# Kernel optimization log

Measured on AMD Instinct MI355X. Metric: run time of the kernel, lower is better.

The kernel has to match this reference:

```python
import jax, jax.numpy as jnp
import numpy as np

BLOCK = 32           # sparsity_config.block
STRIDE_BLOCKS = 4    # stride 128 // block 32
B, H, L, HD = 2, 16, 4096, 64


def _make_fixed_layout(nb, bs):
    """DeepSpeed 'fixed' unidirectional layout, numverts=vertsize=1 (same for all heads)."""
    lay = np.zeros((nb, nb), dtype=np.int64)
    # local: lower-triangular within each stride window
    for i in range(0, nb, bs):
        for j in range(i, i + bs):
            lay[j, i:j + 1] = 1
    # global: vertical stripe at column offset bs-1 of every window, causal (col < row)
    start = bs - 1
    for i in range(nb):
        for j in range(start, i, bs):
            lay[i, j] = 1
    rows, cols = np.nonzero(lay)  # sorted by row
    return jnp.asarray(rows, jnp.int32), jnp.asarray(cols, jnp.int32)


def setup_inputs() -> dict:
    key = jax.random.key(0)
    kq, kk, kv = jax.random.split(key, 3)
    query = jax.random.normal(kq, (B, H, L, HD), jnp.float32)
    key_t = jax.random.normal(kk, (B, H, L, HD), jnp.float32)
    value = jax.random.normal(kv, (B, H, L, HD), jnp.float32)
    rows, cols = _make_fixed_layout(L // BLOCK, STRIDE_BLOCKS)
    return {"query": query, "key": key_t, "value": value,
            "rows": rows, "cols": cols, "block": BLOCK}


def reference(query, key, value, rows, cols, block):
    b, h, l, hd = query.shape
    nb = l // block
    scale = float(hd) ** (-0.5)
    # [nb, B, H, block, hd] with block-row axis leading for gather/scatter
    qb = jnp.moveaxis(query.reshape(b, h, nb, block, hd), 2, 0)
    kb = jnp.moveaxis(key.reshape(b, h, nb, block, hd), 2, 0)
    vb = jnp.moveaxis(value.reshape(b, h, nb, block, hd), 2, 0)
    # sdd: scores only on active blocks -> [nnz, B, H, block, block]
    s = jnp.einsum('nbhqd,nbhkd->nbhqk', qb[rows], kb[cols]) * scale
    # block-sparse softmax over each query row (segment reduce over blocks sharing a row)
    m_blk = s.max(-1)  # [nnz, B, H, block]
    row_max = jnp.full((nb, b, h, block), -jnp.inf, s.dtype).at[rows].max(m_blk)
    e = jnp.exp(s - row_max[rows][..., None])
    denom = jnp.zeros((nb, b, h, block), s.dtype).at[rows].add(e.sum(-1))
    p = e / denom[rows][..., None]
    # dsd: probs @ value, scatter-add into block rows
    ob = jnp.zeros((nb, b, h, block, hd), s.dtype).at[rows].add(
        jnp.einsum('nbhqk,nbhkd->nbhqd', p, vb[cols]))
    return jnp.moveaxis(ob, 0, 2).reshape(b, h, l, hd)
```

## Files before the change

kernel.cpp:

```cpp
#include <hip/hip_runtime.h>
#include <math.h>

#define BH    32
#define LSEQ  4096
#define HD    64
#define BLK   32
#define NB    128
#define NWIN  32
#define QSCALE 0.18033688011112042f

#define KSTR 34
#define VSTR 17

#define RAW_BARRIER() asm volatile("s_waitcnt lgkmcnt(0)\n\ts_barrier" ::: "memory")

typedef _Float16 h2  __attribute__((ext_vector_type(2)));
typedef _Float16 h8  __attribute__((ext_vector_type(8)));
typedef float    f16v __attribute__((ext_vector_type(16)));

static __device__ __forceinline__ h2 pk(float a, float b) {
    return __builtin_bit_cast(h2, __builtin_amdgcn_cvt_pkrtz(a, b));
}
static __device__ __forceinline__ unsigned pku(float a, float b) {
    return __builtin_bit_cast(unsigned, __builtin_amdgcn_cvt_pkrtz(a, b));
}
static __device__ __forceinline__ short h16(float x) {
    return __builtin_bit_cast(short, (_Float16)x);
}
static __device__ __forceinline__ h8 mk8(h2 a, h2 b, h2 c, h2 d) {
    h8 r;
    r[0] = a[0]; r[1] = a[1]; r[2] = b[0]; r[3] = b[1];
    r[4] = c[0]; r[5] = c[1]; r[6] = d[0]; r[7] = d[1];
    return r;
}

__global__ __launch_bounds__(256)
void sparse_attn_noshfl(const float* __restrict__ Q, const float* __restrict__ K,
                        const float* __restrict__ V, float* __restrict__ out)
{
    const int id = (int)blockIdx.x;
    const int bh = id & 31;
    const int p  = id >> 5;

    const int t    = (int)threadIdx.x;
    const int d    = t >> 6;
    const int lane = t & 63;
    const int l31  = lane & 31;
    const int h    = lane >> 5;

    __shared__ __align__(16) unsigned kbuf[2][BLK * KSTR];
    __shared__ __align__(16) unsigned vbuf[2][HD * VSTR];

    const size_t base = (size_t)bh * (LSEQ * HD);

    const int srow = t >> 3;
    const int sdg  = t & 7;
    const int vslot = (srow & 19) | ((srow & 4) << 1) | ((srow & 8) >> 1);

    const float* kgb = K + base + (size_t)srow * HD + sdg * 8;
    const float* vgb = V + base + (size_t)srow * HD + sdg * 8;

    float4 kA, kB, vA, vB;

    auto loadR = [&](int w, int j) {
        const int col = (j < w) ? (4 * j + 3) : (4 * w + (j - w));
        const size_t off = (size_t)col * (BLK * HD);
        kA = *(const float4*)(kgb + off);
        kB = *(const float4*)(kgb + off + 4);
        vA = *(const float4*)(vgb + off);
        vB = *(const float4*)(vgb + off + 4);
    };
    auto writeL = [&](int b) {
        uint2 w0, w1;
        w0.x = pku(kA.x, kA.y); w0.y = pku(kA.z, kA.w);
        w1.x = pku(kB.x, kB.y); w1.y = pku(kB.z, kB.w);
        *(uint2*)&kbuf[b][srow * KSTR + sdg * 4]     = w0;
        *(uint2*)&kbuf[b][srow * KSTR + sdg * 4 + 2] = w1;
        short* vs = (short*)&vbuf[b][0];
        const int vd0 = sdg * 8;
        vs[(vd0 + 0) * (2 * VSTR) + vslot] = h16(vA.x);
        vs[(vd0 + 1) * (2 * VSTR) + vslot] = h16(vA.y);
        vs[(vd0 + 2) * (2 * VSTR) + vslot] = h16(vA.z);
        vs[(vd0 + 3) * (2 * VSTR) + vslot] = h16(vA.w);
        vs[(vd0 + 4) * (2 * VSTR) + vslot] = h16(vB.x);
        vs[(vd0 + 5) * (2 * VSTR) + vslot] = h16(vB.y);
        vs[(vd0 + 6) * (2 * VSTR) + vslot] = h16(vB.z);
        vs[(vd0 + 7) * (2 * VSTR) + vslot] = h16(vB.w);
    };

    int pb = 0;
    loadR(p, 0);

    for (int ph = 0; ph < 2; ++ph) {
        const int w = ph ? (31 - p) : p;
        const int r = 4 * w + d;
        const int n = w + 4;

        const float* qp = Q + base + (size_t)(r * BLK + l31) * HD + 8 * h;
        h8 qf[4];
#pragma unroll
        for (int tt = 0; tt < 4; ++tt) {
            float4 a = *(const float4*)(qp + 16 * tt);
            float4 b = *(const float4*)(qp + 16 * tt + 4);
            qf[tt] = mk8(pk(a.x * QSCALE, a.y * QSCALE), pk(a.z * QSCALE, a.w * QSCALE),
                         pk(b.x * QSCALE, b.y * QSCALE), pk(b.z * QSCALE, b.w * QSCALE));
        }

        f16v o0 = {}, o1 = {};
        float2 ls2 = make_float2(0.0f, 0.0f);

        for (int j = 0; j < n; ++j, pb ^= 1) {
            writeL(pb);
            if (j + 1 < n)      loadR(w, j + 1);
            else if (ph == 0)   loadR(31 - p, 0);
            RAW_BARRIER();

            if (j < w || (j - w) <= d) {
                const unsigned* kb = kbuf[pb];
                const unsigned* vb = vbuf[pb];

                f16v st = {};
#pragma unroll
                for (int tt = 0; tt < 4; ++tt) {
                    const int kw = l31 * KSTR + 8 * tt + 4 * h;
                    uint2 u0 = *(const uint2*)&kb[kw];
                    uint2 u1 = *(const uint2*)&kb[kw + 2];
                    uint4 uu; uu.x = u0.x; uu.y = u0.y; uu.z = u1.x; uu.w = u1.y;
                    h8 kf = __builtin_bit_cast(h8, uu);
                    st = __builtin_amdgcn_mfma_f32_32x32x16_f16(kf, qf[tt], st, 0, 0, 0);
                }

                float ps[16];
#pragma unroll
                for (int g = 0; g < 16; ++g) ps[g] = __builtin_exp2f(st[g]);
#pragma unroll
                for (int g = 0; g < 8; ++g) {
                    ls2.x += ps[2 * g];
                    ls2.y += ps[2 * g + 1];
                }
                h2 ph2[8];
#pragma unroll
                for (int jj = 0; jj < 8; ++jj) ph2[jj] = pk(ps[2 * jj], ps[2 * jj + 1]);

#pragma unroll
                for (int t2 = 0; t2 < 2; ++t2) {
                    h8 pa = mk8(ph2[4 * t2], ph2[4 * t2 + 1],
                                ph2[4 * t2 + 2], ph2[4 * t2 + 3]);

                    const int va0 = l31 * VSTR + 8 * t2 + 4 * h;
                    const int va1 = (32 + l31) * VSTR + 8 * t2 + 4 * h;
                    uint4 u0, u1;
                    u0.x = vb[va0]; u0.y = vb[va0 + 1]; u0.z = vb[va0 + 2]; u0.w = vb[va0 + 3];
                    u1.x = vb[va1]; u1.y = vb[va1 + 1]; u1.z = vb[va1 + 2]; u1.w = vb[va1 + 3];
                    h8 vf0 = __builtin_bit_cast(h8, u0);
                    h8 vf1 = __builtin_bit_cast(h8, u1);
                    o0 = __builtin_amdgcn_mfma_f32_32x32x16_f16(pa, vf0, o0, 0, 0, 0);
                    o1 = __builtin_amdgcn_mfma_f32_32x32x16_f16(pa, vf1, o1, 0, 0, 0);
                }
            }
        }

        float lsum = ls2.x + ls2.y;
        lsum += __shfl_xor(lsum, 32);
        const float inv = 1.0f / lsum;

        float* op = out + base + (size_t)(r * BLK) * HD;
#pragma unroll
        for (int g = 0; g < 16; ++g) {
            const int qrow = (g & 3) + 8 * (g >> 2) + 4 * h;
            int iv = __builtin_amdgcn_ds_bpermute(qrow << 2, __float_as_int(inv));
            const float invq = __int_as_float(iv);
            op[(size_t)qrow * HD + l31]      = o0[g] * invq;
            op[(size_t)qrow * HD + 32 + l31] = o1[g] * invq;
        }
    }
}

extern "C" void kernel_launch(void* const* d_in, const int* in_sizes, int n_in,
                              void* d_out, int out_size, void* d_ws, size_t ws_size,
                              hipStream_t stream) {
    const float* Q = (const float*)d_in[0];
    const float* K = (const float*)d_in[1];
    const float* V = (const float*)d_in[2];

    dim3 grid(NWIN * BH / 2);
    dim3 block(256);
    sparse_attn_noshfl<<<grid, block, 0, stream>>>(Q, K, V, (float*)d_out);
}
```

Baseline: 178.7 us.

## Flatten two-window loop into single pipelined loop with register-prefetched LDS fragments

Merges the two per-block window phases into one flat 39-iteration loop, with both windows' Q fragments and accumulators held in registers at once. Each iteration first reads the K/V fragments from LDS into registers, then writes the next tile to the other buffer and issues the global load two tiles ahead, then runs the MFMAs. This deepens the global-load prefetch to distance two and overlaps LDS staging with compute. In exchange it raises register pressure from the doubled accumulators and Q fragments, which may reduce occupancy.

New measurement: 164.6 us. 7.9% less time.

```diff
diff --git a/kernel.cpp b/kernel.cpp
--- a/kernel.cpp
+++ b/kernel.cpp
@@ -35,8 +35,8 @@
 }
 
 __global__ __launch_bounds__(256)
-void sparse_attn_noshfl(const float* __restrict__ Q, const float* __restrict__ K,
-                        const float* __restrict__ V, float* __restrict__ out)
+void sparse_attn_rf(const float* __restrict__ Q, const float* __restrict__ K,
+                    const float* __restrict__ V, float* __restrict__ out)
 {
     const int id = (int)blockIdx.x;
     const int bh = id & 31;
@@ -53,6 +53,10 @@
 
     const size_t base = (size_t)bh * (LSEQ * HD);
 
+    const int wA = p, wB = 31 - p;
+    const int nA = wA + 4;
+    const int rA = 4 * wA + d, rB = 4 * wB + d;
+
     const int srow = t >> 3;
     const int sdg  = t & 7;
     const int vslot = (srow & 19) | ((srow & 4) << 1) | ((srow & 8) >> 1);
@@ -62,9 +66,14 @@
 
     float4 kA, kB, vA, vB;
 
-    auto loadR = [&](int w, int j) {
-        const int col = (j < w) ? (4 * j + 3) : (4 * w + (j - w));
-        const size_t off = (size_t)col * (BLK * HD);
+    auto colFlat = [&](int bb) -> int {
+        int w_, j;
+        if (bb < nA) { w_ = wA; j = bb; }
+        else         { w_ = wB; j = bb - nA; }
+        return (j < w_) ? (4 * j + 3) : (4 * w_ + (j - w_));
+    };
+    auto loadR = [&](int bb) {
+        const size_t off = (size_t)colFlat(bb) * (BLK * HD);
         kA = *(const float4*)(kgb + off);
         kB = *(const float4*)(kgb + off + 4);
         vA = *(const float4*)(vgb + off);
@@ -88,82 +97,111 @@
         vs[(vd0 + 7) * (2 * VSTR) + vslot] = h16(vB.w);
     };
 
+    h8 qfA[4], qfB[4];
+    {
+        const float* qpA = Q + base + (size_t)(rA * BLK + l31) * HD + 8 * h;
+        const float* qpB = Q + base + (size_t)(rB * BLK + l31) * HD + 8 * h;
+#pragma unroll
+        for (int tt = 0; tt < 4; ++tt) {
+            float4 a = *(const float4*)(qpA + 16 * tt);
+            float4 b = *(const float4*)(qpA + 16 * tt + 4);
+            qfA[tt] = mk8(pk(a.x * QSCALE, a.y * QSCALE), pk(a.z * QSCALE, a.w * QSCALE),
+                          pk(b.x * QSCALE, b.y * QSCALE), pk(b.z * QSCALE, b.w * QSCALE));
+            float4 c = *(const float4*)(qpB + 16 * tt);
+            float4 e = *(const float4*)(qpB + 16 * tt + 4);
+            qfB[tt] = mk8(pk(c.x * QSCALE, c.y * QSCALE), pk(c.z * QSCALE, c.w * QSCALE),
+                          pk(e.x * QSCALE, e.y * QSCALE), pk(e.z * QSCALE, e.w * QSCALE));
+        }
+    }
+
+    f16v oA0 = {}, oA1 = {}, oB0 = {}, oB1 = {};
+    float2 lsA = make_float2(0.0f, 0.0f);
+    float2 lsB = make_float2(0.0f, 0.0f);
+
+    loadR(0);
+    writeL(0);
+    loadR(1);
+    RAW_BARRIER();
     int pb = 0;
-    loadR(p, 0);
-
-    for (int ph = 0; ph < 2; ++ph) {
-        const int w = ph ? (31 - p) : p;
-        const int r = 4 * w + d;
-        const int n = w + 4;
-
-        const float* qp = Q + base + (size_t)(r * BLK + l31) * HD + 8 * h;
-        h8 qf[4];
-#pragma unroll
-        for (int tt = 0; tt < 4; ++tt) {
-            float4 a = *(const float4*)(qp + 16 * tt);
-            float4 b = *(const float4*)(qp + 16 * tt + 4);
-            qf[tt] = mk8(pk(a.x * QSCALE, a.y * QSCALE), pk(a.z * QSCALE, a.w * QSCALE),
-                         pk(b.x * QSCALE, b.y * QSCALE), pk(b.z * QSCALE, b.w * QSCALE));
-        }
-
-        f16v o0 = {}, o1 = {};
-        float2 ls2 = make_float2(0.0f, 0.0f);
-
-        for (int j = 0; j < n; ++j, pb ^= 1) {
-            writeL(pb);
-            if (j + 1 < n)      loadR(w, j + 1);
-            else if (ph == 0)   loadR(31 - p, 0);
-            RAW_BARRIER();
-
-            if (j < w || (j - w) <= d) {
-                const unsigned* kb = kbuf[pb];
-                const unsigned* vb = vbuf[pb];
-
+
+    for (int bb = 0; bb < 39; ++bb, pb ^= 1) {
+        const bool phB = bb >= nA;
+        const int  w_  = phB ? wB : wA;
+        const int  j   = phB ? (bb - nA) : bb;
+        const bool act = (j < w_) || ((j - w_) <= d);
+
+        const unsigned* kb = kbuf[pb];
+        const unsigned* vb = vbuf[pb];
+
+        uint4 kr0, kr1, kr2, kr3, vr00, vr01, vr10, vr11;
+        if (act) {
+            const int kw = l31 * KSTR + 4 * h;
+            {
+                uint2 a = *(const uint2*)&kb[kw +  0], b = *(const uint2*)&kb[kw +  2];
+                kr0.x = a.x; kr0.y = a.y; kr0.z = b.x; kr0.w = b.y;
+            }
+            {
+                uint2 a = *(const uint2*)&kb[kw +  8], b = *(const uint2*)&kb[kw + 10];
+                kr1.x = a.x; kr1.y = a.y; kr1.z = b.x; kr1.w = b.y;
+            }
+            {
+                uint2 a = *(const uint2*)&kb[kw + 16], b = *(const uint2*)&kb[kw + 18];
+                kr2.x = a.x; kr2.y = a.y; kr2.z = b.x; kr2.w = b.y;
+            }
+            {
+                uint2 a = *(const uint2*)&kb[kw + 24], b = *(const uint2*)&kb[kw + 26];
+                kr3.x = a.x; kr3.y = a.y; kr3.z = b.x; kr3.w = b.y;
+            }
+            const int va0 = l31 * VSTR + 4 * h;
+            const int va1 = (32 + l31) * VSTR + 4 * h;
+            vr00.x = vb[va0];      vr00.y = vb[va0 + 1];  vr00.z = vb[va0 + 2];  vr00.w = vb[va0 + 3];
+            vr10.x = vb[va0 + 8];  vr10.y = vb[va0 + 9];  vr10.z = vb[va0 + 10]; vr10.w = vb[va0 + 11];
+            vr01.x = vb[va1];      vr01.y = vb[va1 + 1];  vr01.z = vb[va1 + 2];  vr01.w = vb[va1 + 3];
+            vr11.x = vb[va1 + 8];  vr11.y = vb[va1 + 9];  vr11.z = vb[va1 + 10]; vr11.w = vb[va1 + 11];
+        }
+        __builtin_amdgcn_sched_barrier(0);
+
+        if (bb + 1 < 39) writeL(pb ^ 1);
+        if (bb + 2 < 39) loadR(bb + 2);
+
+        if (act) {
+            auto tile = [&](const h8 (&qf)[4], f16v& o0, f16v& o1, float2& ls) {
                 f16v st = {};
-#pragma unroll
-                for (int tt = 0; tt < 4; ++tt) {
-                    const int kw = l31 * KSTR + 8 * tt + 4 * h;
-                    uint2 u0 = *(const uint2*)&kb[kw];
-                    uint2 u1 = *(const uint2*)&kb[kw + 2];
-                    uint4 uu; uu.x = u0.x; uu.y = u0.y; uu.z = u1.x; uu.w = u1.y;
-                    h8 kf = __builtin_bit_cast(h8, uu);
-                    st = __builtin_amdgcn_mfma_f32_32x32x16_f16(kf, qf[tt], st, 0, 0, 0);
-                }
+                st = __builtin_amdgcn_mfma_f32_32x32x16_f16(__builtin_bit_cast(h8, kr0), qf[0], st, 0, 0, 0);
+                st = __builtin_amdgcn_mfma_f32_32x32x16_f16(__builtin_bit_cast(h8, kr1), qf[1], st, 0, 0, 0);
+                st = __builtin_amdgcn_mfma_f32_32x32x16_f16(__builtin_bit_cast(h8, kr2), qf[2], st, 0, 0, 0);
+                st = __builtin_amdgcn_mfma_f32_32x32x16_f16(__builtin_bit_cast(h8, kr3), qf[3], st, 0, 0, 0);
 
                 float ps[16];
 #pragma unroll
                 for (int g = 0; g < 16; ++g) ps[g] = __builtin_exp2f(st[g]);
 #pragma unroll
                 for (int g = 0; g < 8; ++g) {
-                    ls2.x += ps[2 * g];
-                    ls2.y += ps[2 * g + 1];
+                    ls.x += ps[2 * g];
+                    ls.y += ps[2 * g + 1];
                 }
                 h2 ph2[8];
 #pragma unroll
-                for (int jj = 0; jj < 8; ++jj) ph2[jj] = pk(ps[2 * jj], ps[2 * jj + 1]);
-
-#pragma unroll
-                for (int t2 = 0; t2 < 2; ++t2) {
-                    h8 pa = mk8(ph2[4 * t2], ph2[4 * t2 + 1],
-                                ph2[4 * t2 + 2], ph2[4 * t2 + 3]);
-
-                    const int va0 = l31 * VSTR + 8 * t2 + 4 * h;
-                    const int va1 = (32 + l31) * VSTR + 8 * t2 + 4 * h;
-                    uint4 u0, u1;
-                    u0.x = vb[va0]; u0.y = vb[va0 + 1]; u0.z = vb[va0 + 2]; u0.w = vb[va0 + 3];
-                    u1.x = vb[va1]; u1.y = vb[va1 + 1]; u1.z = vb[va1 + 2]; u1.w = vb[va1 + 3];
-                    h8 vf0 = __builtin_bit_cast(h8, u0);
-                    h8 vf1 = __builtin_bit_cast(h8, u1);
-                    o0 = __builtin_amdgcn_mfma_f32_32x32x16_f16(pa, vf0, o0, 0, 0, 0);
-                    o1 = __builtin_amdgcn_mfma_f32_32x32x16_f16(pa, vf1, o1, 0, 0, 0);
-                }
-            }
-        }
-
-        float lsum = ls2.x + ls2.y;
+                for (int m = 0; m < 8; ++m) ph2[m] = pk(ps[2 * m], ps[2 * m + 1]);
+
+                h8 pa0 = mk8(ph2[0], ph2[1], ph2[2], ph2[3]);
+                h8 pa1 = mk8(ph2[4], ph2[5], ph2[6], ph2[7]);
+                o0 = __builtin_amdgcn_mfma_f32_32x32x16_f16(pa0, __builtin_bit_cast(h8, vr00), o0, 0, 0, 0);
+                o1 = __builtin_amdgcn_mfma_f32_32x32x16_f16(pa0, __builtin_bit_cast(h8, vr01), o1, 0, 0, 0);
+                o0 = __builtin_amdgcn_mfma_f32_32x32x16_f16(pa1, __builtin_bit_cast(h8, vr10), o0, 0, 0, 0);
+                o1 = __builtin_amdgcn_mfma_f32_32x32x16_f16(pa1, __builtin_bit_cast(h8, vr11), o1, 0, 0, 0);
+            };
+            if (!phB) tile(qfA, oA0, oA1, lsA);
+            else      tile(qfB, oB0, oB1, lsB);
+        }
+
+        RAW_BARRIER();
+    }
+
+    auto finish = [&](float2 ls, const f16v& o0, const f16v& o1, int r) {
+        float lsum = ls.x + ls.y;
         lsum += __shfl_xor(lsum, 32);
         const float inv = 1.0f / lsum;
-
         float* op = out + base + (size_t)(r * BLK) * HD;
 #pragma unroll
         for (int g = 0; g < 16; ++g) {
@@ -173,7 +211,9 @@
             op[(size_t)qrow * HD + l31]      = o0[g] * invq;
             op[(size_t)qrow * HD + 32 + l31] = o1[g] * invq;
         }
-    }
+    };
+    finish(lsA, oA0, oA1, rA);
+    finish(lsB, oB0, oB1, rB);
 }
 
 extern "C" void kernel_launch(void* const* d_in, const int* in_sizes, int n_in,
@@ -185,5 +225,5 @@
 
     dim3 grid(NWIN * BH / 2);
     dim3 block(256);
-    sparse_attn_noshfl<<<grid, block, 0, stream>>>(Q, K, V, (float*)d_out);
-}
+    sparse_attn_rf<<<grid, block, 0, stream>>>(Q, K, V, (float*)d_out);
+}
```
